# Performance work log

Measured on AMD Instinct MI355X. Metric: run time of the kernel, lower is better.

Reference implementation:

```python
import jax, jax.numpy as jnp
import numpy as np

B, L, LM_DIM, D, R, NUM_LAYERS, C = 32, 1024, 1024, 128, 3, 2, 8
N = B * L
E = 524288
LN_EPS = 1e-5


def setup_inputs() -> dict:
    key = jax.random.key(0)
    ks = jax.random.split(key, 16)
    inp = {
        'output': jax.random.normal(ks[0], (B, L, LM_DIM), dtype=jnp.float32),
        'edge_index': jax.random.randint(ks[1], (2, E), 0, N, dtype=jnp.int64),
        'edge_type': jax.random.randint(ks[2], (E,), 0, R, dtype=jnp.int64),
        'attention_mask': jax.random.randint(ks[3], (B, L), 0, 2, dtype=jnp.int64),
        'labels': jax.random.randint(ks[4], (B, L), 0, C, dtype=jnp.int64),
        # parameters
        'lm_W': jax.random.normal(ks[5], (D, LM_DIM), dtype=jnp.float32) * 0.02,
        'lm_b': jnp.zeros((D,), dtype=jnp.float32),
        'ln_g': jnp.ones((D,), dtype=jnp.float32),
        'ln_b': jnp.zeros((D,), dtype=jnp.float32),
        'W_rel': jax.random.normal(ks[6], (NUM_LAYERS, R, D, D), dtype=jnp.float32) * 0.05,
        'W_root': jax.random.normal(ks[7], (NUM_LAYERS, D, D), dtype=jnp.float32) * 0.05,
        'conv_b': jnp.zeros((NUM_LAYERS, D), dtype=jnp.float32),
        'cls_W': jax.random.normal(ks[8], (C, 2 * D), dtype=jnp.float32) * 0.05,
        'cls_b': jnp.zeros((C,), dtype=jnp.float32),
    }
    return inp


def _forward(output, edge_index, edge_type, attention_mask, labels,
             lm_W, lm_b, ln_g, ln_b, W_rel, W_root, conv_b, cls_W, cls_b):
    # LM head + ReLU (dropout is identity in eval) + LayerNorm
    lm = jax.nn.relu(jnp.einsum('bld,hd->blh', output, lm_W) + lm_b)
    mu = jnp.mean(lm, axis=-1, keepdims=True)
    var = jnp.mean(jnp.square(lm - mu), axis=-1, keepdims=True)
    lm = (lm - mu) * jax.lax.rsqrt(var + LN_EPS) * ln_g + ln_b  # [B,L,D]

    # RGCN over flattened nodes
    x = lm.reshape(N, D)
    src, dst = edge_index[0], edge_index[1]
    seg = dst * R + edge_type  # combined (node, relation) segment id
    ones = jnp.ones((E,), dtype=x.dtype)
    cnt = jax.ops.segment_sum(ones, seg, num_segments=N * R).reshape(N, R, 1)
    denom = jnp.maximum(cnt, 1.0)
    for layer in range(NUM_LAYERS):
        x_src = x[src]  # [E,D] gather
        sums = jax.ops.segment_sum(x_src, seg, num_segments=N * R).reshape(N, R, D)
        mean_r = sums / denom  # per-relation mean aggregation (PyG RGCNConv aggr='mean')
        out = jnp.einsum('nrd,rde->ne', mean_r, W_rel[layer])
        out = out + x @ W_root[layer] + conv_b[layer]
        x = jax.nn.relu(out)  # dropout identity

    g = x.reshape(B, L, D)
    feat = jnp.concatenate([lm, g], axis=-1)  # [B,L,2D]
    logits = jnp.einsum('blh,ch->blc', feat, cls_W) + cls_b  # [B,L,C]

    # masked cross-entropy (ignore where attention_mask != 1)
    valid = (attention_mask.reshape(-1) == 1)
    logp = jax.nn.log_softmax(logits.reshape(-1, C), axis=-1)
    nll = -jnp.take_along_axis(logp, labels.reshape(-1, 1), axis=1)[:, 0]
    n_valid = jnp.maximum(jnp.sum(valid.astype(logits.dtype)), 1.0)
    loss = jnp.sum(jnp.where(valid, nll, 0.0)) / n_valid
    return loss, logits


def reference(output, edge_index, edge_type, attention_mask, labels,
              lm_W, lm_b, ln_g, ln_b, W_rel, W_root, conv_b, cls_W, cls_b):
    return _forward(output, edge_index, edge_type, attention_mask, labels,
                    lm_W, lm_b, ln_g, ln_b, W_rel, W_root, conv_b, cls_W, cls_b)
```

## Files before the change

kernel.cpp:

```cpp
#include <hip/hip_runtime.h>

#define Bb 32
#define Ll 1024
#define LMD 1024
#define Dd 128
#define Rr 3
#define NLAYER 2
#define Cc 8
#define Nn (Bb*Ll)
#define Ee 524288
#define NSEG (Nn*Rr)
#define CAP 64
#define NBLK 512
#define LN_EPS 1e-5f

typedef __attribute__((ext_vector_type(8))) short bf16x8;
typedef __attribute__((ext_vector_type(4))) float f32x4;

__device__ inline short f2bf(float f) {
    unsigned u = __builtin_bit_cast(unsigned, f);
    u += 0x7fff + ((u >> 16) & 1);
    return (short)(u >> 16);
}
__device__ inline float bf2f(unsigned short s) {
    unsigned u = ((unsigned)s) << 16;
    return __builtin_bit_cast(float, u);
}

__global__ __launch_bounds__(256) void prep_kernel(
    const float* __restrict__ lmW, const float* __restrict__ Wrel,
    const float* __restrict__ Wroot, short* __restrict__ Wp_all,
    const int* __restrict__ src, const int* __restrict__ dst,
    const int* __restrict__ et,
    int* __restrict__ fill, int* __restrict__ slots)
{
    int bid = blockIdx.x;
    if (bid < 1024) {
        int idx = bid * 256 + threadIdx.x;
        float v;
        if (idx < 131072) {
            int kk = idx & 31, n = (idx >> 5) & 127, ks = idx >> 12;
            v = lmW[n * 1024 + ks * 32 + kk];
        } else {
            int j = idx - 131072;
            int layer = j >> 16;
            int kk = j & 31, n = (j >> 5) & 127, ks = (j >> 12) & 15;
            int k = ks * 32 + kk;
            v = (k < 384) ? Wrel[(size_t)layer * 49152 + (size_t)k * 128 + n]
                          : Wroot[(size_t)layer * 16384 + (size_t)(k - 384) * 128 + n];
        }
        Wp_all[idx] = f2bf(v);
    } else {
        int e = (bid - 1024) * 256 + threadIdx.x;
        int s = dst[e] * 3 + et[e];
        int pos = atomicAdd(&fill[s], 1);
        if (pos < CAP) slots[(size_t)s * CAP + pos] = src[e];
    }
}

__global__ __launch_bounds__(256) void lm_gemm_ln_kernel(
    const float* __restrict__ A,
    const short* __restrict__ Wp,
    const float* __restrict__ bias,
    const float* __restrict__ lng, const float* __restrict__ lnb,
    short* __restrict__ lm_bf16)
{
    const int wv   = threadIdx.x >> 6;
    const int lane = threadIdx.x & 63;
    const int m16  = lane & 15;
    const int quad = lane >> 4;
    const int row_frag = blockIdx.x * 64 + wv * 16 + m16;
    const float* arow = A + (size_t)row_frag * 1024 + quad * 8;

    f32x4 acc[8];
    #pragma unroll
    for (int i = 0; i < 8; ++i) acc[i] = (f32x4){0.f, 0.f, 0.f, 0.f};

    #pragma unroll 2
    for (int ks = 0; ks < 32; ++ks) {
        const short* wpb = Wp + ks * 4096 + m16 * 32 + quad * 8;
        bf16x8 bfr[8];
        #pragma unroll
        for (int nt = 0; nt < 8; ++nt)
            bfr[nt] = *(const bf16x8*)(wpb + nt * 512);
        const float4* ap = (const float4*)(arow + ks * 32);
        float4 a0 = ap[0], a1 = ap[1];
        union { bf16x8 v; short s[8]; } af;
        af.s[0] = f2bf(a0.x); af.s[1] = f2bf(a0.y);
        af.s[2] = f2bf(a0.z); af.s[3] = f2bf(a0.w);
        af.s[4] = f2bf(a1.x); af.s[5] = f2bf(a1.y);
        af.s[6] = f2bf(a1.z); af.s[7] = f2bf(a1.w);
        #pragma unroll
        for (int nt = 0; nt < 8; ++nt)
            acc[nt] = __builtin_amdgcn_mfma_f32_16x16x32_bf16(af.v, bfr[nt], acc[nt], 0, 0, 0);
    }

    float v[8][4];
    #pragma unroll
    for (int nt = 0; nt < 8; ++nt) {
        float bs = bias[nt * 16 + m16];
        #pragma unroll
        for (int r = 0; r < 4; ++r) v[nt][r] = fmaxf(acc[nt][r] + bs, 0.f);
    }
    float gv[8], bv[8];
    #pragma unroll
    for (int nt = 0; nt < 8; ++nt) { gv[nt] = lng[nt * 16 + m16]; bv[nt] = lnb[nt * 16 + m16]; }

    const int row0 = blockIdx.x * 64 + wv * 16 + quad * 4;
    #pragma unroll
    for (int r = 0; r < 4; ++r) {
        float s = 0.f;
        #pragma unroll
        for (int nt = 0; nt < 8; ++nt) s += v[nt][r];
        s += __shfl_xor(s, 1, 64); s += __shfl_xor(s, 2, 64);
        s += __shfl_xor(s, 4, 64); s += __shfl_xor(s, 8, 64);
        float mu = s * (1.f / 128.f);
        float q = 0.f;
        #pragma unroll
        for (int nt = 0; nt < 8; ++nt) { float d = v[nt][r] - mu; q += d * d; }
        q += __shfl_xor(q, 1, 64); q += __shfl_xor(q, 2, 64);
        q += __shfl_xor(q, 4, 64); q += __shfl_xor(q, 8, 64);
        float rs = rsqrtf(q * (1.f / 128.f) + LN_EPS);
        size_t rowoff = (size_t)(row0 + r) * 128;
        #pragma unroll
        for (int nt = 0; nt < 8; ++nt) {
            float o = (v[nt][r] - mu) * rs * gv[nt] + bv[nt];
            lm_bf16[rowoff + nt * 16 + m16] = f2bf(o);
        }
    }
}

__global__ __launch_bounds__(256) void conv_gemm_kernel(
    const short* __restrict__ A1,
    const short* __restrict__ A2,
    const short* __restrict__ Wp,
    const float* __restrict__ bias,
    short* __restrict__ out_bf16)
{
    const int wv   = threadIdx.x >> 6;
    const int lane = threadIdx.x & 63;
    const int m16  = lane & 15;
    const int quad = lane >> 4;
    const int row_frag = blockIdx.x * 64 + wv * 16 + m16;
    const short* a1row = A1 + (size_t)row_frag * 384 + quad * 8;
    const short* a2row = A2 + (size_t)row_frag * 128 + quad * 8;

    f32x4 acc[8];
    #pragma unroll
    for (int i = 0; i < 8; ++i) acc[i] = (f32x4){0.f, 0.f, 0.f, 0.f};

    #pragma unroll 2
    for (int ks = 0; ks < 16; ++ks) {
        const short* wpb = Wp + ks * 4096 + m16 * 32 + quad * 8;
        bf16x8 bfr[8];
        #pragma unroll
        for (int nt = 0; nt < 8; ++nt)
            bfr[nt] = *(const bf16x8*)(wpb + nt * 512);
        const short* ar = (ks < 12) ? (a1row + ks * 32) : (a2row + (ks - 12) * 32);
        bf16x8 af = *(const bf16x8*)ar;
        #pragma unroll
        for (int nt = 0; nt < 8; ++nt)
            acc[nt] = __builtin_amdgcn_mfma_f32_16x16x32_bf16(af, bfr[nt], acc[nt], 0, 0, 0);
    }

    const int row0 = blockIdx.x * 64 + wv * 16 + quad * 4;
    #pragma unroll
    for (int nt = 0; nt < 8; ++nt) {
        float bs = bias[nt * 16 + m16];
        #pragma unroll
        for (int r = 0; r < 4; ++r) {
            float o = fmaxf(acc[nt][r] + bs, 0.f);
            out_bf16[(size_t)(row0 + r) * 128 + nt * 16 + m16] = f2bf(o);
        }
    }
}

__global__ __launch_bounds__(256) void conv2_cls_kernel(
    const short* __restrict__ A1,
    const short* __restrict__ A2,
    const short* __restrict__ Wp,
    const float* __restrict__ bias,
    const float* __restrict__ clsW, const float* __restrict__ clsb,
    const short* __restrict__ lm,
    const int* __restrict__ mask, const int* __restrict__ labels,
    float* __restrict__ logits, float2* __restrict__ partials)
{
    __shared__ float W[2048];
    __shared__ float2 wred[4];
    for (int i = threadIdx.x; i < 2048; i += 256) W[i] = clsW[i];

    const int wv   = threadIdx.x >> 6;
    const int lane = threadIdx.x & 63;
    const int m16  = lane & 15;
    const int quad = lane >> 4;
    const int row_frag = blockIdx.x * 64 + wv * 16 + m16;
    const short* a1row = A1 + (size_t)row_frag * 384 + quad * 8;
    const short* a2row = A2 + (size_t)row_frag * 128 + quad * 8;

    f32x4 acc[8];
    #pragma unroll
    for (int i = 0; i < 8; ++i) acc[i] = (f32x4){0.f, 0.f, 0.f, 0.f};

    #pragma unroll 2
    for (int ks = 0; ks < 16; ++ks) {
        const short* wpb = Wp + ks * 4096 + m16 * 32 + quad * 8;
        bf16x8 bfr[8];
        #pragma unroll
        for (int nt = 0; nt < 8; ++nt)
            bfr[nt] = *(const bf16x8*)(wpb + nt * 512);
        const short* ar = (ks < 12) ? (a1row + ks * 32) : (a2row + (ks - 12) * 32);
        bf16x8 af = *(const bf16x8*)ar;
        #pragma unroll
        for (int nt = 0; nt < 8; ++nt)
            acc[nt] = __builtin_amdgcn_mfma_f32_16x16x32_bf16(af, bfr[nt], acc[nt], 0, 0, 0);
    }

    float g[8][4];
    #pragma unroll
    for (int nt = 0; nt < 8; ++nt) {
        float bs = bias[nt * 16 + m16];
        #pragma unroll
        for (int r = 0; r < 4; ++r) g[nt][r] = fmaxf(acc[nt][r] + bs, 0.f);
    }

    __syncthreads();

    const int row0 = blockIdx.x * 64 + wv * 16 + quad * 4;
    float lv = 0.f, cv = 0.f;

    #pragma unroll
    for (int r = 0; r < 4; ++r) {
        const int row = row0 + r;
        uint4 raw = *(const uint4*)(lm + (size_t)row * 128 + m16 * 8);
        float a[8];
        a[0] = bf2f((unsigned short)(raw.x & 0xffff)); a[1] = bf2f((unsigned short)(raw.x >> 16));
        a[2] = bf2f((unsigned short)(raw.y & 0xffff)); a[3] = bf2f((unsigned short)(raw.y >> 16));
        a[4] = bf2f((unsigned short)(raw.z & 0xffff)); a[5] = bf2f((unsigned short)(raw.z >> 16));
        a[6] = bf2f((unsigned short)(raw.w & 0xffff)); a[7] = bf2f((unsigned short)(raw.w >> 16));

        float p[8];
        #pragma unroll
        for (int c = 0; c < 8; ++c) {
            float s = 0.f;
            const float* w1 = &W[c * 256 + m16 * 8];
            #pragma unroll
            for (int j = 0; j < 8; ++j) s = fmaf(a[j], w1[j], s);
            const float* w2 = &W[c * 256 + 128 + m16];
            #pragma unroll
            for (int nt = 0; nt < 8; ++nt) s = fmaf(g[nt][r], w2[nt * 16], s);
            p[c] = s;
        }
        #pragma unroll
        for (int c = 0; c < 8; ++c) {
            p[c] += __shfl_xor(p[c], 1, 64); p[c] += __shfl_xor(p[c], 2, 64);
            p[c] += __shfl_xor(p[c], 4, 64); p[c] += __shfl_xor(p[c], 8, 64);
            p[c] += clsb[c];
        }
        if (m16 < 8) {
            float o = p[0];
            #pragma unroll
            for (int c = 1; c < 8; ++c) o = (m16 == c) ? p[c] : o;
            logits[(size_t)row * 8 + m16] = o;
        }
        float mx = p[0];
        #pragma unroll
        for (int c = 1; c < 8; ++c) mx = fmaxf(mx, p[c]);
        float ss = 0.f;
        #pragma unroll
        for (int c = 0; c < 8; ++c) ss += expf(p[c] - mx);
        float lse = mx + logf(ss);
        int y = labels[row];
        float ly = p[0];
        #pragma unroll
        for (int c = 1; c < 8; ++c) ly = (y == c) ? p[c] : ly;
        bool valid = (mask[row] == 1);
        if (m16 == 0 && valid) { lv += lse - ly; cv += 1.f; }
    }

    #pragma unroll
    for (int off = 32; off > 0; off >>= 1) {
        lv += __shfl_down(lv, off, 64);
        cv += __shfl_down(cv, off, 64);
    }
    if (lane == 0) wred[wv] = make_float2(lv, cv);
    __syncthreads();
    if (threadIdx.x == 0) {
        float2 p0 = wred[0], p1 = wred[1], p2 = wred[2], p3 = wred[3];
        partials[blockIdx.x] = make_float2(p0.x + p1.x + p2.x + p3.x,
                                           p0.y + p1.y + p2.y + p3.y);
    }
}

__global__ __launch_bounds__(256) void loss_finalize_kernel(
    const float2* __restrict__ partials, float* __restrict__ loss_out)
{
    __shared__ float2 ws4[4];
    int t = threadIdx.x;
    float lv = 0.f, cv = 0.f;
    for (int i = t; i < NBLK; i += 256) { float2 p = partials[i]; lv += p.x; cv += p.y; }
    #pragma unroll
    for (int off = 32; off > 0; off >>= 1) {
        lv += __shfl_down(lv, off, 64);
        cv += __shfl_down(cv, off, 64);
    }
    if ((t & 63) == 0) ws4[t >> 6] = make_float2(lv, cv);
    __syncthreads();
    if (t == 0) {
        float ls = ws4[0].x + ws4[1].x + ws4[2].x + ws4[3].x;
        float cs = ws4[0].y + ws4[1].y + ws4[2].y + ws4[3].y;
        loss_out[0] = ls / fmaxf(cs, 1.f);
    }
}

__global__ __launch_bounds__(256) void aggregate_kernel(
    const short* __restrict__ x, const int* __restrict__ fill,
    const int* __restrict__ slots, short* __restrict__ agg)
{
    int seg  = blockIdx.x * 4 + (threadIdx.x >> 6);
    int lane = threadIdx.x & 63;
    int grp  = lane >> 4;
    int c    = lane & 15;
    int cnt = fill[seg];
    int e = cnt > CAP ? CAP : cnt;
    int n = seg / 3, r = seg - n * 3;
    const int* sl = slots + (size_t)seg * CAP;

    float a[8];
    #pragma unroll
    for (int j = 0; j < 8; ++j) a[j] = 0.f;

    for (int i = 0; i < e; i += 4) {
        int idx = i + grp;
        if (idx < e) {
            int s0 = sl[idx];
            uint4 u = *(const uint4*)(x + (size_t)s0 * 128 + c * 8);
            a[0] += bf2f((unsigned short)(u.x & 0xffff));
            a[1] += bf2f((unsigned short)(u.x >> 16));
            a[2] += bf2f((unsigned short)(u.y & 0xffff));
            a[3] += bf2f((unsigned short)(u.y >> 16));
            a[4] += bf2f((unsigned short)(u.z & 0xffff));
            a[5] += bf2f((unsigned short)(u.z >> 16));
            a[6] += bf2f((unsigned short)(u.w & 0xffff));
            a[7] += bf2f((unsigned short)(u.w >> 16));
        }
    }

    #pragma unroll
    for (int j = 0; j < 8; ++j) {
        a[j] += __shfl_xor(a[j], 16, 64);
        a[j] += __shfl_xor(a[j], 32, 64);
    }

    if (grp == 0) {
        float inv = 1.f / (float)(cnt > 0 ? cnt : 1);
        union { uint4 u; unsigned short s[8]; } o;
        #pragma unroll
        for (int j = 0; j < 8; ++j) o.s[j] = (unsigned short)f2bf(a[j] * inv);
        *(uint4*)(agg + (size_t)n * 384 + r * 128 + c * 8) = o.u;
    }
}

extern "C" void kernel_launch(void* const* d_in, const int* in_sizes, int n_in,
                              void* d_out, int out_size, void* d_ws, size_t ws_size,
                              hipStream_t stream)
{
    const float* output = (const float*)d_in[0];
    const int* edge_index = (const int*)d_in[1];
    const int* edge_type  = (const int*)d_in[2];
    const int* attn       = (const int*)d_in[3];
    const int* labels     = (const int*)d_in[4];
    const float* lmW   = (const float*)d_in[5];
    const float* lmb   = (const float*)d_in[6];
    const float* lng   = (const float*)d_in[7];
    const float* lnb   = (const float*)d_in[8];
    const float* Wrel  = (const float*)d_in[9];
    const float* Wroot = (const float*)d_in[10];
    const float* convb = (const float*)d_in[11];
    const float* clsW  = (const float*)d_in[12];
    const float* clsb  = (const float*)d_in[13];

    char* ws = (char*)d_ws;
    short* lm_bf  = (short*)ws;                          ws += (size_t)Nn * Dd * 2;
    short* x1_bf  = (short*)ws;                          ws += (size_t)Nn * Dd * 2;
    short* agg_bf = (short*)ws;                          ws += (size_t)Nn * 384 * 2;
    short* Wp_all = (short*)ws;                          ws += (size_t)262144 * 2;
    float2* partials = (float2*)ws;                      ws += (size_t)NBLK * 8;
    int* fill     = (int*)ws;                            ws += (size_t)NSEG * 4;
    int* slots    = (int*)ws;

    short* Wp_lm = Wp_all;
    short* Wp_c0 = Wp_all + 131072;
    short* Wp_c1 = Wp_all + 131072 + 65536;

    const int* e_src = edge_index;
    const int* e_dst = edge_index + Ee;

    hipMemsetAsync(fill, 0, (size_t)NSEG * 4, stream);

    prep_kernel<<<dim3(1024 + Ee / 256), dim3(256), 0, stream>>>(
        lmW, Wrel, Wroot, Wp_all, e_src, e_dst, edge_type, fill, slots);

    lm_gemm_ln_kernel<<<dim3(Nn / 64), dim3(256), 0, stream>>>(
        output, Wp_lm, lmb, lng, lnb, lm_bf);

    aggregate_kernel<<<dim3(NSEG / 4), dim3(256), 0, stream>>>(lm_bf, fill, slots, agg_bf);
    conv_gemm_kernel<<<dim3(Nn / 64), dim3(256), 0, stream>>>(
        agg_bf, lm_bf, Wp_c0, convb, x1_bf);

    aggregate_kernel<<<dim3(NSEG / 4), dim3(256), 0, stream>>>(x1_bf, fill, slots, agg_bf);
    float* logits = (float*)d_out + 1;
    conv2_cls_kernel<<<dim3(Nn / 64), dim3(256), 0, stream>>>(
        agg_bf, x1_bf, Wp_c1, convb + Dd, clsW, clsb, lm_bf,
        attn, labels, logits, partials);

    loss_finalize_kernel<<<dim3(1), dim3(256), 0, stream>>>(partials, (float*)d_out);
}
```

Measured before the change: 424.5 us.

## Fuse neighbor aggregation into conv GEMM kernels via LDS staging

Removes the standalone aggregate kernels and instead has each conv GEMM block gather and average its 64 rows' relation segments into a padded LDS tile, then feed the MFMA loop from LDS. This eliminates the global round-trip of the 384-wide aggregated buffer and two kernel launches. In exchange the latency-bound random gather now runs with far fewer waves (512 blocks, large LDS footprint), reducing memory-level parallelism for the gather phase.

```diff
diff --git a/kernel.cpp b/kernel.cpp
--- a/kernel.cpp
+++ b/kernel.cpp
@@ -12,6 +12,7 @@
 #define NSEG (Nn*Rr)
 #define CAP 64
 #define NBLK 512
+#define LDA 392
 #define LN_EPS 1e-5f
 
 typedef __attribute__((ext_vector_type(8))) short bf16x8;
@@ -130,20 +131,73 @@
     }
 }
 
-__global__ __launch_bounds__(256) void conv_gemm_kernel(
-    const short* __restrict__ A1,
-    const short* __restrict__ A2,
+__device__ inline void block_aggregate_to_lds(
+    const short* __restrict__ x, const int* __restrict__ fill,
+    const int* __restrict__ slots, int row_base, short (*agg_lds)[LDA])
+{
+    const int wv   = threadIdx.x >> 6;
+    const int lane = threadIdx.x & 63;
+    const int grp  = lane >> 4;
+    const int c    = lane & 15;
+    for (int s = wv * 48; s < wv * 48 + 48; ++s) {
+        int localrow = s / 3, r = s - localrow * 3;
+        int seg = (row_base + localrow) * 3 + r;
+        int cnt = fill[seg];
+        int e = cnt > CAP ? CAP : cnt;
+        const int* sl = slots + (size_t)seg * CAP;
+        float a[8];
+        #pragma unroll
+        for (int j = 0; j < 8; ++j) a[j] = 0.f;
+        for (int i = 0; i < e; i += 4) {
+            int idx = i + grp;
+            if (idx < e) {
+                int s0 = sl[idx];
+                uint4 u = *(const uint4*)(x + (size_t)s0 * 128 + c * 8);
+                a[0] += bf2f((unsigned short)(u.x & 0xffff));
+                a[1] += bf2f((unsigned short)(u.x >> 16));
+                a[2] += bf2f((unsigned short)(u.y & 0xffff));
+                a[3] += bf2f((unsigned short)(u.y >> 16));
+                a[4] += bf2f((unsigned short)(u.z & 0xffff));
+                a[5] += bf2f((unsigned short)(u.z >> 16));
+                a[6] += bf2f((unsigned short)(u.w & 0xffff));
+                a[7] += bf2f((unsigned short)(u.w >> 16));
+            }
+        }
+        #pragma unroll
+        for (int j = 0; j < 8; ++j) {
+            a[j] += __shfl_xor(a[j], 16, 64);
+            a[j] += __shfl_xor(a[j], 32, 64);
+        }
+        if (grp == 0) {
+            float inv = 1.f / (float)(cnt > 0 ? cnt : 1);
+            union { uint4 u; unsigned short sh[8]; } o;
+            #pragma unroll
+            for (int j = 0; j < 8; ++j) o.sh[j] = (unsigned short)f2bf(a[j] * inv);
+            *(uint4*)&agg_lds[localrow][r * 128 + c * 8] = o.u;
+        }
+    }
+}
+
+__global__ __launch_bounds__(256) void agg_conv_kernel(
+    const short* __restrict__ x,
+    const int* __restrict__ fill, const int* __restrict__ slots,
     const short* __restrict__ Wp,
     const float* __restrict__ bias,
     short* __restrict__ out_bf16)
 {
+    __shared__ __align__(16) short agg_lds[64][LDA];
+
+    const int row_base = blockIdx.x * 64;
+    block_aggregate_to_lds(x, fill, slots, row_base, agg_lds);
+    __syncthreads();
+
     const int wv   = threadIdx.x >> 6;
     const int lane = threadIdx.x & 63;
     const int m16  = lane & 15;
     const int quad = lane >> 4;
-    const int row_frag = blockIdx.x * 64 + wv * 16 + m16;
-    const short* a1row = A1 + (size_t)row_frag * 384 + quad * 8;
-    const short* a2row = A2 + (size_t)row_frag * 128 + quad * 8;
+    const int row_frag = row_base + wv * 16 + m16;
+    const short* a1row = &agg_lds[wv * 16 + m16][quad * 8];
+    const short* a2row = x + (size_t)row_frag * 128 + quad * 8;
 
     f32x4 acc[8];
     #pragma unroll
@@ -163,7 +217,7 @@
             acc[nt] = __builtin_amdgcn_mfma_f32_16x16x32_bf16(af, bfr[nt], acc[nt], 0, 0, 0);
     }
 
-    const int row0 = blockIdx.x * 64 + wv * 16 + quad * 4;
+    const int row0 = row_base + wv * 16 + quad * 4;
     #pragma unroll
     for (int nt = 0; nt < 8; ++nt) {
         float bs = bias[nt * 16 + m16];
@@ -175,9 +229,9 @@
     }
 }
 
-__global__ __launch_bounds__(256) void conv2_cls_kernel(
-    const short* __restrict__ A1,
-    const short* __restrict__ A2,
+__global__ __launch_bounds__(256) void agg_conv2_cls_kernel(
+    const short* __restrict__ x,
+    const int* __restrict__ fill, const int* __restrict__ slots,
     const short* __restrict__ Wp,
     const float* __restrict__ bias,
     const float* __restrict__ clsW, const float* __restrict__ clsb,
@@ -185,17 +239,22 @@
     const int* __restrict__ mask, const int* __restrict__ labels,
     float* __restrict__ logits, float2* __restrict__ partials)
 {
+    __shared__ __align__(16) short agg_lds[64][LDA];
     __shared__ float W[2048];
     __shared__ float2 wred[4];
     for (int i = threadIdx.x; i < 2048; i += 256) W[i] = clsW[i];
+
+    const int row_base = blockIdx.x * 64;
+    block_aggregate_to_lds(x, fill, slots, row_base, agg_lds);
+    __syncthreads();
 
     const int wv   = threadIdx.x >> 6;
     const int lane = threadIdx.x & 63;
     const int m16  = lane & 15;
     const int quad = lane >> 4;
-    const int row_frag = blockIdx.x * 64 + wv * 16 + m16;
-    const short* a1row = A1 + (size_t)row_frag * 384 + quad * 8;
-    const short* a2row = A2 + (size_t)row_frag * 128 + quad * 8;
+    const int row_frag = row_base + wv * 16 + m16;
+    const short* a1row = &agg_lds[wv * 16 + m16][quad * 8];
+    const short* a2row = x + (size_t)row_frag * 128 + quad * 8;
 
     f32x4 acc[8];
     #pragma unroll
@@ -223,9 +282,7 @@
         for (int r = 0; r < 4; ++r) g[nt][r] = fmaxf(acc[nt][r] + bs, 0.f);
     }
 
-    __syncthreads();
-
-    const int row0 = blockIdx.x * 64 + wv * 16 + quad * 4;
+    const int row0 = row_base + wv * 16 + quad * 4;
     float lv = 0.f, cv = 0.f;
 
     #pragma unroll
@@ -309,54 +366,6 @@
         float ls = ws4[0].x + ws4[1].x + ws4[2].x + ws4[3].x;
         float cs = ws4[0].y + ws4[1].y + ws4[2].y + ws4[3].y;
         loss_out[0] = ls / fmaxf(cs, 1.f);
-    }
-}
-
-__global__ __launch_bounds__(256) void aggregate_kernel(
-    const short* __restrict__ x, const int* __restrict__ fill,
-    const int* __restrict__ slots, short* __restrict__ agg)
-{
-    int seg  = blockIdx.x * 4 + (threadIdx.x >> 6);
-    int lane = threadIdx.x & 63;
-    int grp  = lane >> 4;
-    int c    = lane & 15;
-    int cnt = fill[seg];
-    int e = cnt > CAP ? CAP : cnt;
-    int n = seg / 3, r = seg - n * 3;
-    const int* sl = slots + (size_t)seg * CAP;
-
-    float a[8];
-    #pragma unroll
-    for (int j = 0; j < 8; ++j) a[j] = 0.f;
-
-    for (int i = 0; i < e; i += 4) {
-        int idx = i + grp;
-        if (idx < e) {
-            int s0 = sl[idx];
-            uint4 u = *(const uint4*)(x + (size_t)s0 * 128 + c * 8);
-            a[0] += bf2f((unsigned short)(u.x & 0xffff));
-            a[1] += bf2f((unsigned short)(u.x >> 16));
-            a[2] += bf2f((unsigned short)(u.y & 0xffff));
-            a[3] += bf2f((unsigned short)(u.y >> 16));
-            a[4] += bf2f((unsigned short)(u.z & 0xffff));
-            a[5] += bf2f((unsigned short)(u.z >> 16));
-            a[6] += bf2f((unsigned short)(u.w & 0xffff));
-            a[7] += bf2f((unsigned short)(u.w >> 16));
-        }
-    }
-
-    #pragma unroll
-    for (int j = 0; j < 8; ++j) {
-        a[j] += __shfl_xor(a[j], 16, 64);
-        a[j] += __shfl_xor(a[j], 32, 64);
-    }
-
-    if (grp == 0) {
-        float inv = 1.f / (float)(cnt > 0 ? cnt : 1);
-        union { uint4 u; unsigned short s[8]; } o;
-        #pragma unroll
-        for (int j = 0; j < 8; ++j) o.s[j] = (unsigned short)f2bf(a[j] * inv);
-        *(uint4*)(agg + (size_t)n * 384 + r * 128 + c * 8) = o.u;
     }
 }
 
@@ -382,7 +391,6 @@
     char* ws = (char*)d_ws;
     short* lm_bf  = (short*)ws;                          ws += (size_t)Nn * Dd * 2;
     short* x1_bf  = (short*)ws;                          ws += (size_t)Nn * Dd * 2;
-    short* agg_bf = (short*)ws;                          ws += (size_t)Nn * 384 * 2;
     short* Wp_all = (short*)ws;                          ws += (size_t)262144 * 2;
     float2* partials = (float2*)ws;                      ws += (size_t)NBLK * 8;
     int* fill     = (int*)ws;                            ws += (size_t)NSEG * 4;
@@ -403,14 +411,12 @@
     lm_gemm_ln_kernel<<<dim3(Nn / 64), dim3(256), 0, stream>>>(
         output, Wp_lm, lmb, lng, lnb, lm_bf);
 
-    aggregate_kernel<<<dim3(NSEG / 4), dim3(256), 0, stream>>>(lm_bf, fill, slots, agg_bf);
-    conv_gemm_kernel<<<dim3(Nn / 64), dim3(256), 0, stream>>>(
-        agg_bf, lm_bf, Wp_c0, convb, x1_bf);
-
-    aggregate_kernel<<<dim3(NSEG / 4), dim3(256), 0, stream>>>(x1_bf, fill, slots, agg_bf);
+    agg_conv_kernel<<<dim3(NBLK), dim3(256), 0, stream>>>(
+        lm_bf, fill, slots, Wp_c0, convb, x1_bf);
+
     float* logits = (float*)d_out + 1;
-    conv2_cls_kernel<<<dim3(Nn / 64), dim3(256), 0, stream>>>(
-        agg_bf, x1_bf, Wp_c1, convb + Dd, clsW, clsb, lm_bf,
+    agg_conv2_cls_kernel<<<dim3(NBLK), dim3(256), 0, stream>>>(
+        x1_bf, fill, slots, Wp_c1, convb + Dd, clsW, clsb, lm_bf,
         attn, labels, logits, partials);
 
     loss_finalize_kernel<<<dim3(1), dim3(256), 0, stream>>>(partials, (float*)d_out);
```

New measurement: 500.5 us. 17.9% more time.
